# Kernel optimization log

Measured on AMD Instinct MI355X. Metric: run time of the kernel, lower is better.

Reference implementation:

```python
import jax, jax.numpy as jnp
import numpy as np
import math

NUM_HEADS = 8
HEAD_DIM = 64
MID = NUM_HEADS * HEAD_DIM  # 512
OUT_FEATURES = 512
NUM_BUCKETS = 32            # rel_pos_num_buckets (module passes 2*this to bucket fn)
MAX_DISTANCE = 128
SCALE = HEAD_DIM ** -0.5


def _relative_position_bucket(rel_pos, num_buckets, max_distance):
    # faithful port of RelativePositionBias._relative_position_bucket
    num_buckets = num_buckets // 2
    ret = (rel_pos >= 0).astype(jnp.int32) * num_buckets
    n = jnp.abs(rel_pos)
    max_exact = max(1, num_buckets // 2)
    denom = math.log(max_distance / max_exact) if max_distance > max_exact else 1.0
    n_float = jnp.maximum(n.astype(jnp.float32), 1.0)
    val_if_large = (max_exact + jnp.log(n_float / max_exact) / denom * (num_buckets - max_exact)).astype(jnp.int32)
    val_if_large = jnp.minimum(val_if_large, num_buckets - 1)
    ret = ret + jnp.where(n < max_exact, n, val_if_large)
    return ret


def rel_pos_bias(table, num_q, num_k):
    # table: [2*NUM_BUCKETS, heads] -> bias [1, heads, q, k]
    q_pos = jnp.arange(num_q, dtype=jnp.int32)
    k_pos = jnp.arange(num_k, dtype=jnp.int32)
    rel = k_pos[None, :] - q_pos[:, None]                      # [q, k]
    bucket = _relative_position_bucket(rel, NUM_BUCKETS * 2, MAX_DISTANCE)
    bias = table[bucket]                                       # [q, k, h]
    return jnp.transpose(bias, (2, 0, 1))[None]                # [1, h, q, k]


def setup_inputs() -> dict:
    key = jax.random.key(0)
    ks = jax.random.split(key, 6)
    b, n = 2, 4096
    q = jax.random.normal(ks[0], (b, n, MID), dtype=jnp.float32)
    k = jax.random.normal(ks[1], (b, n, MID), dtype=jnp.float32)
    v = jax.random.normal(ks[2], (b, n, MID), dtype=jnp.float32)
    # bucket indices range over [0, 2*NUM_BUCKETS); size table accordingly
    rel_bias_table = jax.random.normal(ks[3], (2 * NUM_BUCKETS, NUM_HEADS), dtype=jnp.float32) * 0.02
    W_out = jax.random.normal(ks[4], (MID, OUT_FEATURES), dtype=jnp.float32) * (1.0 / math.sqrt(MID))
    b_out = jax.random.normal(ks[5], (OUT_FEATURES,), dtype=jnp.float32) * 0.01
    return {"q": q, "k": k, "v": v, "rel_bias_table": rel_bias_table, "W_out": W_out, "b_out": b_out}


def reference(q, k, v, rel_bias_table, W_out, b_out):
    b, n, _ = q.shape
    m = k.shape[1]
    split = lambda t: jnp.transpose(t.reshape(t.shape[0], t.shape[1], NUM_HEADS, HEAD_DIM), (0, 2, 1, 3))
    qh, kh, vh = split(q), split(k), split(v)                  # [b, h, n, d]
    sim = jnp.einsum('bhnd,bhmd->bhnm', qh, kh)                # [b, h, n, m]
    sim = sim + rel_pos_bias(rel_bias_table, n, m)             # bias added BEFORE scaling (as in source)
    sim = sim * SCALE
    attn = jax.nn.softmax(sim, axis=-1)
    out = jnp.einsum('bhnm,bhmd->bhnd', attn, vh)              # [b, h, n, d]
    out = jnp.transpose(out, (0, 2, 1, 3)).reshape(b, n, MID)  # [b, n, h*d]
    return out @ W_out + b_out
```

## Files before the change

kernel.cpp:

```cpp
#include <hip/hip_runtime.h>
#include <hip/hip_bf16.h>
#include <math.h>

#define BB 2
#define HH 8
#define NN 4096
#define DD 64
#define MID 512
#define NOUT 512
#define QB 128
#define KVT 64
#define NT (NN / KVT)
#define LOG2E 1.44269504088896340736f
#define SCALE 0.125f

typedef __attribute__((ext_vector_type(8)))  short bf16x8;
typedef __attribute__((ext_vector_type(4)))  float f32x4;
typedef __attribute__((ext_vector_type(16))) float f32x16;

__device__ __forceinline__ short f2bf(float x) {
  unsigned u = __builtin_bit_cast(unsigned, x);
  u = (u + 0x7FFFu + ((u >> 16) & 1u)) >> 16;
  return (short)u;
}

__device__ __forceinline__ int rp_bucket(int rel) {
  int ret = (rel >= 0) ? 32 : 0;
  int n = (rel >= 0) ? rel : -rel;
  if (n < 16) return ret + n;
  float nf = (float)n;
  float vf = 16.0f + (logf(nf * (1.0f / 16.0f)) / 2.0794415416798357f) * 16.0f;
  int vi = (int)vf;
  vi = vi < 31 ? vi : 31;
  return ret + vi;
}

__device__ __forceinline__ unsigned cvtpk(float lo, float hi) {
  unsigned d;
  asm("v_cvt_pk_bf16_f32 %0, %1, %2" : "=v"(d) : "v"(lo), "v"(hi));
  return d;
}

__device__ __forceinline__ void gl2lds16(const void* g, void* l) {
  __builtin_amdgcn_global_load_lds(
      (const __attribute__((address_space(1))) unsigned*)g,
      (__attribute__((address_space(3))) unsigned*)l, 16, 0, 0);
}

__global__ void wconv_kernel(const float* __restrict__ W, short* __restrict__ Wt) {
  int i = blockIdx.x * 256 + threadIdx.x;
  int kin = i >> 9, n = i & 511;
  Wt[n * MID + kin] = f2bf(W[i]);
}

__global__ __launch_bounds__(256) void kconv_kernel(const float* __restrict__ K,
                                                    short* __restrict__ Kws) {
  int i = blockIdx.x * 256 + threadIdx.x;
  int a = i & 7;
  int h = (i >> 3) & 7;
  int n = (i >> 6) & 4095;
  int b = i >> 18;
  const float* src = K + ((size_t)(b * 4096 + n) * 512 + h * 64 + a * 8);
  float4 x0 = *(const float4*)src;
  float4 x1 = *(const float4*)(src + 4);
  union { short s[8]; bf16x8 v; } pk;
  pk.s[0] = f2bf(x0.x); pk.s[1] = f2bf(x0.y); pk.s[2] = f2bf(x0.z); pk.s[3] = f2bf(x0.w);
  pk.s[4] = f2bf(x1.x); pk.s[5] = f2bf(x1.y); pk.s[6] = f2bf(x1.z); pk.s[7] = f2bf(x1.w);
  size_t off = ((size_t)(b * 8 + h) * 4096 + n) * 64 + (size_t)((a ^ (n & 7)) * 8);
  *(bf16x8*)(Kws + off) = pk.v;
}

__global__ __launch_bounds__(256) void vconv_kernel(const float* __restrict__ V,
                                                    short* __restrict__ Vtws) {
  __shared__ short Vl[64][72];
  const int t = threadIdx.x;
  const int g = blockIdx.x;
  const int bh = blockIdx.y;
  const int b = bh >> 3, h = bh & 7;
  const int c4 = t & 15, r = t >> 4;
  #pragma unroll
  for (int rr = 0; rr < 4; ++rr) {
    int nl = r + rr * 16;
    const float* src = V + ((size_t)(b * 4096 + g * 64 + nl) * 512 + h * 64 + c4 * 4);
    float4 x = *(const float4*)src;
    Vl[nl][c4 * 4 + 0] = f2bf(x.x);
    Vl[nl][c4 * 4 + 1] = f2bf(x.y);
    Vl[nl][c4 * 4 + 2] = f2bf(x.z);
    Vl[nl][c4 * 4 + 3] = f2bf(x.w);
  }
  __syncthreads();
  #pragma unroll
  for (int it = 0; it < 2; ++it) {
    int u = t + it * 256;
    int d = u >> 3, sp = u & 7;
    int s = sp ^ (d & 7);
    union { short s[8]; bf16x8 v; } pk;
    #pragma unroll
    for (int e = 0; e < 8; ++e) {
      int np  = s * 8 + e;
      int p16 = np & 15;
      int kvl = (np & 48) | (4 * (p16 >> 3) + (p16 & 3) + 8 * ((p16 >> 2) & 1));
      pk.s[e] = Vl[kvl][d];
    }
    *(bf16x8*)(Vtws + ((size_t)bh * 64 + d) * 4096 + g * 64 + sp * 8) = pk.v;
  }
}

__global__ __launch_bounds__(256, 2) void attn_kernel(
    const float* __restrict__ q, const short* __restrict__ kws,
    const short* __restrict__ vtws, const float* __restrict__ table,
    short* __restrict__ attn_out)
{
  __shared__ short Ks[2][4096];
  __shared__ short Vs[2][4096];
  __shared__ float biasb[512];
  __shared__ float Lw[4][32];

  const int tid = threadIdx.x;
  const int w   = tid >> 6;
  const int l   = tid & 63;
  const int lq  = l & 31;
  const int hi  = l >> 5;

  const int raw = blockIdx.x;
  const int bh  = (raw & 7) * 2 + (raw >> 8);
  const int xb  = (raw >> 3) & 31;
  const int b = bh >> 3, h = bh & 7;
  const int q0 = xb * QB;
  const int qw = q0 + w * 32;
  const int qg = qw + lq;

  const float smul = SCALE * LOG2E;

  for (int i = tid; i < 512; i += 256)
    biasb[i] = table[rp_bucket(i - 256) * HH + h] * smul;
  const float c_lo = table[31 * HH + h] * smul;
  const float c_hi = table[63 * HH + h] * smul;

  f32x16 c16h, c16l;
  #pragma unroll
  for (int r = 0; r < 16; ++r) { c16h[r] = c_hi; c16l[r] = c_lo; }

  bf16x8 qf[4];
  {
    const float* qr = q + ((size_t)b * NN + qg) * MID + (size_t)h * DD;
    #pragma unroll
    for (int dc = 0; dc < 4; ++dc) {
      int d0 = dc * 16 + hi * 8;
      float4 a0 = *(const float4*)(qr + d0);
      float4 a1 = *(const float4*)(qr + d0 + 4);
      bf16x8 f;
      f[0] = f2bf(a0.x * smul); f[1] = f2bf(a0.y * smul);
      f[2] = f2bf(a0.z * smul); f[3] = f2bf(a0.w * smul);
      f[4] = f2bf(a1.x * smul); f[5] = f2bf(a1.y * smul);
      f[6] = f2bf(a1.z * smul); f[7] = f2bf(a1.w * smul);
      qf[dc] = f;
    }
  }

  const short* kbh = kws  + (size_t)bh * NN * DD;
  const short* vbh = vtws + (size_t)bh * DD * NN;

  f32x16 o0a = {}, o0b = {}, o1a = {}, o1b = {};
  float ls0 = 0.f, ls1 = 0.f, ls2 = 0.f, ls3 = 0.f;

  const int o1w = w * 1024 + l * 16;
  const int o2w = o1w + 4096;
  const char* pkA = (const char*)kbh + o1w;
  const char* pvA = (const char*)vbh + (size_t)(o1w >> 7) * 8192 + (o1w & 127);
  const char* pvB = (const char*)vbh + (size_t)(o2w >> 7) * 8192 + (o2w & 127);
  char* ldsK = (char*)&Ks[0][0] + w * 1024;
  char* ldsV = (char*)&Vs[0][0] + w * 1024;

#define STAGE(BOFF) {                                   \
    gl2lds16(pkA,        ldsK + (BOFF));                \
    gl2lds16(pkA + 4096, ldsK + (BOFF) + 4096);         \
    gl2lds16(pvA,        ldsV + (BOFF));                \
    gl2lds16(pvB,        ldsV + (BOFF) + 4096);         \
    pkA += 8192; pvA += 128; pvB += 128; }

  STAGE(0);
  __syncthreads();

  for (int t = 0; t < NT; ++t) {
    const int cur = t & 1;
    const int kv0 = t * KVT;
    if (t + 1 < NT) STAGE((cur ^ 1) ? 8192 : 0);

    const char* kr0 = (const char*)&Ks[cur][0] + lq * 128;
    const char* kr1 = kr0 + 32 * 128;
    const int swz = lq & 7;
    bf16x8 kf00 = *(const bf16x8*)(kr0 + ((hi ^ swz) << 4));
    bf16x8 kf10 = *(const bf16x8*)(kr1 + ((hi ^ swz) << 4));

    const int lo_rel = kv0 - (qw + 31);
    const int hi_rel = kv0 + KVT - 1 - qw;
    f32x16 acc0, acc1;
    if (lo_rel > 127) {
      acc0 = __builtin_amdgcn_mfma_f32_32x32x16_bf16(kf00, qf[0], c16h, 0, 0, 0);
      acc1 = __builtin_amdgcn_mfma_f32_32x32x16_bf16(kf10, qf[0], c16h, 0, 0, 0);
    } else if (hi_rel < -127) {
      acc0 = __builtin_amdgcn_mfma_f32_32x32x16_bf16(kf00, qf[0], c16l, 0, 0, 0);
      acc1 = __builtin_amdgcn_mfma_f32_32x32x16_bf16(kf10, qf[0], c16l, 0, 0, 0);
    } else {
      const int bidx0 = kv0 - qg + 256;
      f32x16 g0, g1;
      #pragma unroll
      for (int r = 0; r < 16; ++r) {
        int cr = (r & 3) + 8 * (r >> 2) + 4 * hi;
        g0[r] = biasb[bidx0 + cr];
        g1[r] = biasb[bidx0 + 32 + cr];
      }
      acc0 = __builtin_amdgcn_mfma_f32_32x32x16_bf16(kf00, qf[0], g0, 0, 0, 0);
      acc1 = __builtin_amdgcn_mfma_f32_32x32x16_bf16(kf10, qf[0], g1, 0, 0, 0);
    }
    __builtin_amdgcn_s_setprio(1);
    #pragma unroll
    for (int dc = 1; dc < 4; ++dc) {
      bf16x8 kf0 = *(const bf16x8*)(kr0 + (((dc * 2 + hi) ^ swz) << 4));
      bf16x8 kf1 = *(const bf16x8*)(kr1 + (((dc * 2 + hi) ^ swz) << 4));
      acc0 = __builtin_amdgcn_mfma_f32_32x32x16_bf16(kf0, qf[dc], acc0, 0, 0, 0);
      acc1 = __builtin_amdgcn_mfma_f32_32x32x16_bf16(kf1, qf[dc], acc1, 0, 0, 0);
    }
    __builtin_amdgcn_s_setprio(0);

    float p0[16], p1[16];
    #pragma unroll
    for (int r = 0; r < 16; ++r) p0[r] = __builtin_amdgcn_exp2f(acc0[r]);
    #pragma unroll
    for (int r = 0; r < 16; ++r) p1[r] = __builtin_amdgcn_exp2f(acc1[r]);

    ls0 += ((p0[0] + p0[1]) + (p0[2] + p0[3])) + ((p0[4] + p0[5]) + (p0[6] + p0[7]));
    ls1 += ((p0[8] + p0[9]) + (p0[10] + p0[11])) + ((p0[12] + p0[13]) + (p0[14] + p0[15]));
    ls2 += ((p1[0] + p1[1]) + (p1[2] + p1[3])) + ((p1[4] + p1[5]) + (p1[6] + p1[7]));
    ls3 += ((p1[8] + p1[9]) + (p1[10] + p1[11])) + ((p1[12] + p1[13]) + (p1[14] + p1[15]));

    bf16x8 pa[4];
    {
      union { unsigned u[4]; bf16x8 v; } ua, ub, uc, ud;
      ua.u[0] = cvtpk(p0[0],  p0[1]);  ua.u[1] = cvtpk(p0[2],  p0[3]);
      ua.u[2] = cvtpk(p0[4],  p0[5]);  ua.u[3] = cvtpk(p0[6],  p0[7]);
      ub.u[0] = cvtpk(p0[8],  p0[9]);  ub.u[1] = cvtpk(p0[10], p0[11]);
      ub.u[2] = cvtpk(p0[12], p0[13]); ub.u[3] = cvtpk(p0[14], p0[15]);
      uc.u[0] = cvtpk(p1[0],  p1[1]);  uc.u[1] = cvtpk(p1[2],  p1[3]);
      uc.u[2] = cvtpk(p1[4],  p1[5]);  uc.u[3] = cvtpk(p1[6],  p1[7]);
      ud.u[0] = cvtpk(p1[8],  p1[9]);  ud.u[1] = cvtpk(p1[10], p1[11]);
      ud.u[2] = cvtpk(p1[12], p1[13]); ud.u[3] = cvtpk(p1[14], p1[15]);
      pa[0] = ua.v; pa[1] = ub.v; pa[2] = uc.v; pa[3] = ud.v;
    }

    {
      const char* vb = (const char*)&Vs[cur][0];
      const char* vr0 = vb + lq * 128;
      const char* vr1 = vr0 + 32 * 128;
      const int s0 = lq & 7;
      __builtin_amdgcn_s_setprio(1);
      #pragma unroll
      for (int ks = 0; ks < 4; ks += 2) {
        bf16x8 vfa0 = *(const bf16x8*)(vr0 + (((hi + 2 * ks) ^ s0) << 4));
        bf16x8 vfb0 = *(const bf16x8*)(vr0 + (((hi + 2 * (ks + 1)) ^ s0) << 4));
        bf16x8 vfa1 = *(const bf16x8*)(vr1 + (((hi + 2 * ks) ^ s0) << 4));
        bf16x8 vfb1 = *(const bf16x8*)(vr1 + (((hi + 2 * (ks + 1)) ^ s0) << 4));
        o0a = __builtin_amdgcn_mfma_f32_32x32x16_bf16(pa[ks],     vfa0, o0a, 0, 0, 0);
        o0b = __builtin_amdgcn_mfma_f32_32x32x16_bf16(pa[ks + 1], vfb0, o0b, 0, 0, 0);
        o1a = __builtin_amdgcn_mfma_f32_32x32x16_bf16(pa[ks],     vfa1, o1a, 0, 0, 0);
        o1b = __builtin_amdgcn_mfma_f32_32x32x16_bf16(pa[ks + 1], vfb1, o1b, 0, 0, 0);
      }
      __builtin_amdgcn_s_setprio(0);
    }

    __syncthreads();
  }

  f32x16 o0, o1;
  #pragma unroll
  for (int r = 0; r < 16; ++r) { o0[r] = o0a[r] + o0b[r]; o1[r] = o1a[r] + o1b[r]; }
  float lsum = (ls0 + ls1) + (ls2 + ls3);
  float tot = lsum + __shfl_xor(lsum, 32);
  if (l < 32) Lw[w][l] = tot;
  float inv[16];
  #pragma unroll
  for (int g = 0; g < 4; ++g) {
    f32x4 t4 = *(const f32x4*)&Lw[w][g * 8 + hi * 4];
    inv[g * 4 + 0] = 1.0f / t4[0];
    inv[g * 4 + 1] = 1.0f / t4[1];
    inv[g * 4 + 2] = 1.0f / t4[2];
    inv[g * 4 + 3] = 1.0f / t4[3];
  }
  const size_t ob = ((size_t)b * NN + qw) * MID + (size_t)h * DD;
  #pragma unroll
  for (int r = 0; r < 16; ++r) {
    const int crow = (r & 3) + 8 * (r >> 2) + 4 * hi;
    short* orow = attn_out + ob + (size_t)crow * MID;
    orow[lq]      = f2bf(o0[r] * inv[r]);
    orow[32 + lq] = f2bf(o1[r] * inv[r]);
  }
#undef STAGE
}

__global__ __launch_bounds__(256) void proj_kernel(
    const short* __restrict__ A, const short* __restrict__ Wt,
    const float* __restrict__ bias, float* __restrict__ out)
{
  const int tid = threadIdx.x;
  const int w  = tid >> 6;
  const int l  = tid & 63;
  const int lr = l & 15;
  const int lg = l >> 4;
  const int m0 = blockIdx.x * 64 + w * 16;
  const int n0 = blockIdx.y * 64;

  f32x4 acc[4] = {};
  const short* ar = A + (size_t)(m0 + lr) * MID + lg * 8;
  #pragma unroll
  for (int kk = 0; kk < MID; kk += 32) {
    bf16x8 af = *(const bf16x8*)(ar + kk);
    #pragma unroll
    for (int u = 0; u < 4; ++u) {
      bf16x8 bfr = *(const bf16x8*)(Wt + (size_t)(n0 + u * 16 + lr) * MID + kk + lg * 8);
      acc[u] = __builtin_amdgcn_mfma_f32_16x16x32_bf16(af, bfr, acc[u], 0, 0, 0);
    }
  }
  #pragma unroll
  for (int u = 0; u < 4; ++u) {
    float bb = bias[n0 + u * 16 + lr];
    #pragma unroll
    for (int r = 0; r < 4; ++r)
      out[(size_t)(m0 + lg * 4 + r) * NOUT + n0 + u * 16 + lr] = acc[u][r] + bb;
  }
}

extern "C" void kernel_launch(void* const* d_in, const int* in_sizes, int n_in,
                              void* d_out, int out_size, void* d_ws, size_t ws_size,
                              hipStream_t stream) {
  const float* q     = (const float*)d_in[0];
  const float* k     = (const float*)d_in[1];
  const float* v     = (const float*)d_in[2];
  const float* table = (const float*)d_in[3];
  const float* W     = (const float*)d_in[4];
  const float* bo    = (const float*)d_in[5];
  float* out = (float*)d_out;

  char* wsp = (char*)d_ws;
  short* attn_ws = (short*)wsp;                       wsp += (size_t)BB * NN * MID * 2;
  short* Wt      = (short*)wsp;                       wsp += (size_t)MID * NOUT * 2;
  short* kws     = (short*)wsp;                       wsp += (size_t)BB * HH * NN * DD * 2;
  short* vtws    = (short*)wsp;

  hipLaunchKernelGGL(wconv_kernel, dim3(MID * NOUT / 256), dim3(256), 0, stream, W, Wt);
  hipLaunchKernelGGL(kconv_kernel, dim3(BB * HH * NN * DD / 8 / 256), dim3(256), 0, stream, k, kws);
  hipLaunchKernelGGL(vconv_kernel, dim3(NN / 64, BB * HH), dim3(256), 0, stream, v, vtws);
  hipLaunchKernelGGL(attn_kernel, dim3(BB * HH * (NN / QB)), dim3(256), 0, stream,
                     q, kws, vtws, table, attn_ws);
  hipLaunchKernelGGL(proj_kernel, dim3(BB * NN / 64, NOUT / 64), dim3(256), 0, stream,
                     attn_ws, Wt, bo, out);
}
```

Measured before the change: 140.4 us.

## Split KV across wave pairs with smaller query blocks and LDS reduction

Halves the query block to 64 rows, so each block has two wave pairs. Each pair handles a different 32-key half of every 64-key stage, with both pairs sharing the 32 query rows per wave. This doubles the number of blocks and raises the occupancy hint to 4 blocks per CU, with smaller per-wave accumulators. The partial outputs and row sums from the two pairs are combined through LDS at the end. The V transpose layout and its swizzle change to match the 32-key sub-tiles. In exchange, each K/V tile serves fewer query rows, so global and LDS traffic per output rises, and an extra reduction with syncs is added.

```diff
diff --git a/kernel.cpp b/kernel.cpp
--- a/kernel.cpp
+++ b/kernel.cpp
@@ -8,9 +8,9 @@
 #define DD 64
 #define MID 512
 #define NOUT 512
-#define QB 128
-#define KVT 64
-#define NT (NN / KVT)
+#define QB 64
+#define KVT 32
+#define NSS 64
 #define LOG2E 1.44269504088896340736f
 #define SCALE 0.125f
 
@@ -93,11 +93,12 @@
   for (int it = 0; it < 2; ++it) {
     int u = t + it * 256;
     int d = u >> 3, sp = u & 7;
-    int s = sp ^ (d & 7);
+    int chunk = sp >> 2;
+    int sl = (sp & 3) ^ (d & 3);
     union { short s[8]; bf16x8 v; } pk;
     #pragma unroll
     for (int e = 0; e < 8; ++e) {
-      int np  = s * 8 + e;
+      int np  = chunk * 32 + sl * 8 + e;
       int p16 = np & 15;
       int kvl = (np & 48) | (4 * (p16 >> 3) + (p16 & 3) + 8 * ((p16 >> 2) & 1));
       pk.s[e] = Vl[kvl][d];
@@ -106,13 +107,13 @@
   }
 }
 
-__global__ __launch_bounds__(256, 2) void attn_kernel(
+__global__ __launch_bounds__(256, 4) void attn_kernel(
     const float* __restrict__ q, const short* __restrict__ kws,
     const short* __restrict__ vtws, const float* __restrict__ table,
     short* __restrict__ attn_out)
 {
-  __shared__ short Ks[2][4096];
-  __shared__ short Vs[2][4096];
+  __shared__ short Ks[2][2][2048];
+  __shared__ short Vs[2][2][2048];
   __shared__ float biasb[512];
   __shared__ float Lw[4][32];
 
@@ -121,13 +122,15 @@
   const int l   = tid & 63;
   const int lq  = l & 31;
   const int hi  = l >> 5;
+  const int p   = w >> 1;
+  const int qs  = (w & 1) * 32;
 
   const int raw = blockIdx.x;
-  const int bh  = (raw & 7) * 2 + (raw >> 8);
-  const int xb  = (raw >> 3) & 31;
+  const int bh  = (raw & 7) * 2 + (raw >> 9);
+  const int xb  = (raw >> 3) & 63;
   const int b = bh >> 3, h = bh & 7;
   const int q0 = xb * QB;
-  const int qw = q0 + w * 32;
+  const int qw = q0 + qs;
   const int qg = qw + lq;
 
   const float smul = SCALE * LOG2E;
@@ -158,114 +161,87 @@
     }
   }
 
-  const short* kbh = kws  + (size_t)bh * NN * DD;
-  const short* vbh = vtws + (size_t)bh * DD * NN;
+  const char* kbh = (const char*)(kws  + (size_t)bh * NN * DD);
+  const char* vbh = (const char*)(vtws + (size_t)bh * DD * NN);
 
   f32x16 o0a = {}, o0b = {}, o1a = {}, o1b = {};
-  float ls0 = 0.f, ls1 = 0.f, ls2 = 0.f, ls3 = 0.f;
-
-  const int o1w = w * 1024 + l * 16;
-  const int o2w = o1w + 4096;
-  const char* pkA = (const char*)kbh + o1w;
-  const char* pvA = (const char*)vbh + (size_t)(o1w >> 7) * 8192 + (o1w & 127);
-  const char* pvB = (const char*)vbh + (size_t)(o2w >> 7) * 8192 + (o2w & 127);
-  char* ldsK = (char*)&Ks[0][0] + w * 1024;
-  char* ldsV = (char*)&Vs[0][0] + w * 1024;
-
-#define STAGE(BOFF) {                                   \
-    gl2lds16(pkA,        ldsK + (BOFF));                \
-    gl2lds16(pkA + 4096, ldsK + (BOFF) + 4096);         \
-    gl2lds16(pvA,        ldsV + (BOFF));                \
-    gl2lds16(pvB,        ldsV + (BOFF) + 4096);         \
-    pkA += 8192; pvA += 128; pvB += 128; }
-
-  STAGE(0);
+  float ls0 = 0.f, ls1 = 0.f;
+
+  const char* pk = kbh + tid * 16;
+  const char* pv = vbh + (size_t)(tid >> 2) * 8192 + (tid & 3) * 16;
+
+#define STAGE(BUF, SS) {                                                    \
+    gl2lds16(pk + (size_t)(SS) * 8192,        (char*)&Ks[BUF][0][0] + w * 1024); \
+    gl2lds16(pk + (size_t)(SS) * 8192 + 4096, (char*)&Ks[BUF][1][0] + w * 1024); \
+    gl2lds16(pv + (SS) * 128,                 (char*)&Vs[BUF][0][0] + w * 1024); \
+    gl2lds16(pv + (SS) * 128 + 64,            (char*)&Vs[BUF][1][0] + w * 1024); }
+
+  STAGE(0, 0);
   __syncthreads();
 
-  for (int t = 0; t < NT; ++t) {
-    const int cur = t & 1;
-    const int kv0 = t * KVT;
-    if (t + 1 < NT) STAGE((cur ^ 1) ? 8192 : 0);
-
-    const char* kr0 = (const char*)&Ks[cur][0] + lq * 128;
-    const char* kr1 = kr0 + 32 * 128;
+  for (int ss = 0; ss < NSS; ++ss) {
+    const int cur = ss & 1;
+    if (ss + 1 < NSS) STAGE(cur ^ 1, ss + 1);
+
+    const int kv0 = ss * 64 + p * 32;
+
+    const char* kr = (const char*)&Ks[cur][p][0] + lq * 128;
     const int swz = lq & 7;
-    bf16x8 kf00 = *(const bf16x8*)(kr0 + ((hi ^ swz) << 4));
-    bf16x8 kf10 = *(const bf16x8*)(kr1 + ((hi ^ swz) << 4));
+    bf16x8 kf0 = *(const bf16x8*)(kr + ((hi ^ swz) << 4));
 
     const int lo_rel = kv0 - (qw + 31);
     const int hi_rel = kv0 + KVT - 1 - qw;
-    f32x16 acc0, acc1;
+    f32x16 acc;
     if (lo_rel > 127) {
-      acc0 = __builtin_amdgcn_mfma_f32_32x32x16_bf16(kf00, qf[0], c16h, 0, 0, 0);
-      acc1 = __builtin_amdgcn_mfma_f32_32x32x16_bf16(kf10, qf[0], c16h, 0, 0, 0);
+      acc = __builtin_amdgcn_mfma_f32_32x32x16_bf16(kf0, qf[0], c16h, 0, 0, 0);
     } else if (hi_rel < -127) {
-      acc0 = __builtin_amdgcn_mfma_f32_32x32x16_bf16(kf00, qf[0], c16l, 0, 0, 0);
-      acc1 = __builtin_amdgcn_mfma_f32_32x32x16_bf16(kf10, qf[0], c16l, 0, 0, 0);
+      acc = __builtin_amdgcn_mfma_f32_32x32x16_bf16(kf0, qf[0], c16l, 0, 0, 0);
     } else {
       const int bidx0 = kv0 - qg + 256;
-      f32x16 g0, g1;
+      f32x16 g0;
       #pragma unroll
-      for (int r = 0; r < 16; ++r) {
-        int cr = (r & 3) + 8 * (r >> 2) + 4 * hi;
-        g0[r] = biasb[bidx0 + cr];
-        g1[r] = biasb[bidx0 + 32 + cr];
-      }
-      acc0 = __builtin_amdgcn_mfma_f32_32x32x16_bf16(kf00, qf[0], g0, 0, 0, 0);
-      acc1 = __builtin_amdgcn_mfma_f32_32x32x16_bf16(kf10, qf[0], g1, 0, 0, 0);
+      for (int r = 0; r < 16; ++r)
+        g0[r] = biasb[bidx0 + ((r & 3) + 8 * (r >> 2) + 4 * hi)];
+      acc = __builtin_amdgcn_mfma_f32_32x32x16_bf16(kf0, qf[0], g0, 0, 0, 0);
     }
     __builtin_amdgcn_s_setprio(1);
     #pragma unroll
     for (int dc = 1; dc < 4; ++dc) {
-      bf16x8 kf0 = *(const bf16x8*)(kr0 + (((dc * 2 + hi) ^ swz) << 4));
-      bf16x8 kf1 = *(const bf16x8*)(kr1 + (((dc * 2 + hi) ^ swz) << 4));
-      acc0 = __builtin_amdgcn_mfma_f32_32x32x16_bf16(kf0, qf[dc], acc0, 0, 0, 0);
-      acc1 = __builtin_amdgcn_mfma_f32_32x32x16_bf16(kf1, qf[dc], acc1, 0, 0, 0);
+      bf16x8 kf = *(const bf16x8*)(kr + (((dc * 2 + hi) ^ swz) << 4));
+      acc = __builtin_amdgcn_mfma_f32_32x32x16_bf16(kf, qf[dc], acc, 0, 0, 0);
     }
     __builtin_amdgcn_s_setprio(0);
 
-    float p0[16], p1[16];
-    #pragma unroll
-    for (int r = 0; r < 16; ++r) p0[r] = __builtin_amdgcn_exp2f(acc0[r]);
-    #pragma unroll
-    for (int r = 0; r < 16; ++r) p1[r] = __builtin_amdgcn_exp2f(acc1[r]);
-
+    float p0[16];
+    #pragma unroll
+    for (int r = 0; r < 16; ++r) p0[r] = __builtin_amdgcn_exp2f(acc[r]);
     ls0 += ((p0[0] + p0[1]) + (p0[2] + p0[3])) + ((p0[4] + p0[5]) + (p0[6] + p0[7]));
     ls1 += ((p0[8] + p0[9]) + (p0[10] + p0[11])) + ((p0[12] + p0[13]) + (p0[14] + p0[15]));
-    ls2 += ((p1[0] + p1[1]) + (p1[2] + p1[3])) + ((p1[4] + p1[5]) + (p1[6] + p1[7]));
-    ls3 += ((p1[8] + p1[9]) + (p1[10] + p1[11])) + ((p1[12] + p1[13]) + (p1[14] + p1[15]));
-
-    bf16x8 pa[4];
+
+    bf16x8 pa0, pa1;
     {
-      union { unsigned u[4]; bf16x8 v; } ua, ub, uc, ud;
+      union { unsigned u[4]; bf16x8 v; } ua, ub;
       ua.u[0] = cvtpk(p0[0],  p0[1]);  ua.u[1] = cvtpk(p0[2],  p0[3]);
       ua.u[2] = cvtpk(p0[4],  p0[5]);  ua.u[3] = cvtpk(p0[6],  p0[7]);
       ub.u[0] = cvtpk(p0[8],  p0[9]);  ub.u[1] = cvtpk(p0[10], p0[11]);
       ub.u[2] = cvtpk(p0[12], p0[13]); ub.u[3] = cvtpk(p0[14], p0[15]);
-      uc.u[0] = cvtpk(p1[0],  p1[1]);  uc.u[1] = cvtpk(p1[2],  p1[3]);
-      uc.u[2] = cvtpk(p1[4],  p1[5]);  uc.u[3] = cvtpk(p1[6],  p1[7]);
-      ud.u[0] = cvtpk(p1[8],  p1[9]);  ud.u[1] = cvtpk(p1[10], p1[11]);
-      ud.u[2] = cvtpk(p1[12], p1[13]); ud.u[3] = cvtpk(p1[14], p1[15]);
-      pa[0] = ua.v; pa[1] = ub.v; pa[2] = uc.v; pa[3] = ud.v;
+      pa0 = ua.v; pa1 = ub.v;
     }
 
     {
-      const char* vb = (const char*)&Vs[cur][0];
-      const char* vr0 = vb + lq * 128;
-      const char* vr1 = vr0 + 32 * 128;
-      const int s0 = lq & 7;
+      const char* vb  = (const char*)&Vs[cur][p][0];
+      const char* vr0 = vb + lq * 64;
+      const char* vr1 = vb + (32 + lq) * 64;
+      const int s0 = lq & 3;
       __builtin_amdgcn_s_setprio(1);
-      #pragma unroll
-      for (int ks = 0; ks < 4; ks += 2) {
-        bf16x8 vfa0 = *(const bf16x8*)(vr0 + (((hi + 2 * ks) ^ s0) << 4));
-        bf16x8 vfb0 = *(const bf16x8*)(vr0 + (((hi + 2 * (ks + 1)) ^ s0) << 4));
-        bf16x8 vfa1 = *(const bf16x8*)(vr1 + (((hi + 2 * ks) ^ s0) << 4));
-        bf16x8 vfb1 = *(const bf16x8*)(vr1 + (((hi + 2 * (ks + 1)) ^ s0) << 4));
-        o0a = __builtin_amdgcn_mfma_f32_32x32x16_bf16(pa[ks],     vfa0, o0a, 0, 0, 0);
-        o0b = __builtin_amdgcn_mfma_f32_32x32x16_bf16(pa[ks + 1], vfb0, o0b, 0, 0, 0);
-        o1a = __builtin_amdgcn_mfma_f32_32x32x16_bf16(pa[ks],     vfa1, o1a, 0, 0, 0);
-        o1b = __builtin_amdgcn_mfma_f32_32x32x16_bf16(pa[ks + 1], vfb1, o1b, 0, 0, 0);
-      }
+      bf16x8 va0 = *(const bf16x8*)(vr0 + ((hi ^ s0) << 4));
+      bf16x8 vb0 = *(const bf16x8*)(vr0 + (((hi + 2) ^ s0) << 4));
+      bf16x8 va1 = *(const bf16x8*)(vr1 + ((hi ^ s0) << 4));
+      bf16x8 vb1 = *(const bf16x8*)(vr1 + (((hi + 2) ^ s0) << 4));
+      o0a = __builtin_amdgcn_mfma_f32_32x32x16_bf16(pa0, va0, o0a, 0, 0, 0);
+      o0b = __builtin_amdgcn_mfma_f32_32x32x16_bf16(pa1, vb0, o0b, 0, 0, 0);
+      o1a = __builtin_amdgcn_mfma_f32_32x32x16_bf16(pa0, va1, o1a, 0, 0, 0);
+      o1b = __builtin_amdgcn_mfma_f32_32x32x16_bf16(pa1, vb1, o1b, 0, 0, 0);
       __builtin_amdgcn_s_setprio(0);
     }
 
@@ -275,25 +251,42 @@
   f32x16 o0, o1;
   #pragma unroll
   for (int r = 0; r < 16; ++r) { o0[r] = o0a[r] + o0b[r]; o1[r] = o1a[r] + o1b[r]; }
-  float lsum = (ls0 + ls1) + (ls2 + ls3);
+  float lsum = ls0 + ls1;
   float tot = lsum + __shfl_xor(lsum, 32);
   if (l < 32) Lw[w][l] = tot;
-  float inv[16];
-  #pragma unroll
-  for (int g = 0; g < 4; ++g) {
-    f32x4 t4 = *(const f32x4*)&Lw[w][g * 8 + hi * 4];
-    inv[g * 4 + 0] = 1.0f / t4[0];
-    inv[g * 4 + 1] = 1.0f / t4[1];
-    inv[g * 4 + 2] = 1.0f / t4[2];
-    inv[g * 4 + 3] = 1.0f / t4[3];
-  }
-  const size_t ob = ((size_t)b * NN + qw) * MID + (size_t)h * DD;
-  #pragma unroll
-  for (int r = 0; r < 16; ++r) {
-    const int crow = (r & 3) + 8 * (r >> 2) + 4 * hi;
-    short* orow = attn_out + ob + (size_t)crow * MID;
-    orow[lq]      = f2bf(o0[r] * inv[r]);
-    orow[32 + lq] = f2bf(o1[r] * inv[r]);
+
+  float* Olds = (float*)&Ks[0][0][0];
+  __syncthreads();
+  if (w >= 2) {
+    float* ob = Olds + (w & 1) * 2048;
+    #pragma unroll
+    for (int r = 0; r < 16; ++r) {
+      const int crow = (r & 3) + 8 * (r >> 2) + 4 * hi;
+      ob[crow * 64 + lq]      = o0[r];
+      ob[crow * 64 + 32 + lq] = o1[r];
+    }
+  }
+  __syncthreads();
+  if (w < 2) {
+    float inv[16];
+    #pragma unroll
+    for (int g = 0; g < 4; ++g) {
+      f32x4 ta = *(const f32x4*)&Lw[w][g * 8 + hi * 4];
+      f32x4 tb = *(const f32x4*)&Lw[w + 2][g * 8 + hi * 4];
+      inv[g * 4 + 0] = 1.0f / (ta[0] + tb[0]);
+      inv[g * 4 + 1] = 1.0f / (ta[1] + tb[1]);
+      inv[g * 4 + 2] = 1.0f / (ta[2] + tb[2]);
+      inv[g * 4 + 3] = 1.0f / (ta[3] + tb[3]);
+    }
+    const float* ob = Olds + (w & 1) * 2048;
+    const size_t obase = ((size_t)b * NN + qw) * MID + (size_t)h * DD;
+    #pragma unroll
+    for (int r = 0; r < 16; ++r) {
+      const int crow = (r & 3) + 8 * (r >> 2) + 4 * hi;
+      short* orow = attn_out + obase + (size_t)crow * MID;
+      orow[lq]      = f2bf((o0[r] + ob[crow * 64 + lq])      * inv[r]);
+      orow[32 + lq] = f2bf((o1[r] + ob[crow * 64 + 32 + lq]) * inv[r]);
+    }
   }
 #undef STAGE
 }
```

Result: slower. 444.7 us (+216.8%).

## Triple-buffer K/V tiles with one barrier per step and fuse prep kernels

Applied to the files above, without the earlier changes.

The attention loop moves from double to triple buffering of K/V tiles in LDS. It waits with explicit vmcnt counts and uses a single barrier per iteration, while the load for tile t+2 is issued after compute. The three conversion kernels (W transpose, K swizzle, V transpose) are merged into one launch dispatched by block index, cutting launch overhead. The cost is 16 KB more LDS per block, which may reduce occupancy from the two blocks per CU requested by the launch bounds. It also relies on the hand-written vmcnt accounting being right.

```diff
diff --git a/kernel.cpp b/kernel.cpp
--- a/kernel.cpp
+++ b/kernel.cpp
@@ -47,62 +47,64 @@
       (__attribute__((address_space(3))) unsigned*)l, 16, 0, 0);
 }
 
-__global__ void wconv_kernel(const float* __restrict__ W, short* __restrict__ Wt) {
-  int i = blockIdx.x * 256 + threadIdx.x;
-  int kin = i >> 9, n = i & 511;
-  Wt[n * MID + kin] = f2bf(W[i]);
-}
-
-__global__ __launch_bounds__(256) void kconv_kernel(const float* __restrict__ K,
-                                                    short* __restrict__ Kws) {
-  int i = blockIdx.x * 256 + threadIdx.x;
-  int a = i & 7;
-  int h = (i >> 3) & 7;
-  int n = (i >> 6) & 4095;
-  int b = i >> 18;
-  const float* src = K + ((size_t)(b * 4096 + n) * 512 + h * 64 + a * 8);
-  float4 x0 = *(const float4*)src;
-  float4 x1 = *(const float4*)(src + 4);
-  union { short s[8]; bf16x8 v; } pk;
-  pk.s[0] = f2bf(x0.x); pk.s[1] = f2bf(x0.y); pk.s[2] = f2bf(x0.z); pk.s[3] = f2bf(x0.w);
-  pk.s[4] = f2bf(x1.x); pk.s[5] = f2bf(x1.y); pk.s[6] = f2bf(x1.z); pk.s[7] = f2bf(x1.w);
-  size_t off = ((size_t)(b * 8 + h) * 4096 + n) * 64 + (size_t)((a ^ (n & 7)) * 8);
-  *(bf16x8*)(Kws + off) = pk.v;
-}
-
-__global__ __launch_bounds__(256) void vconv_kernel(const float* __restrict__ V,
-                                                    short* __restrict__ Vtws) {
-  __shared__ short Vl[64][72];
-  const int t = threadIdx.x;
-  const int g = blockIdx.x;
-  const int bh = blockIdx.y;
-  const int b = bh >> 3, h = bh & 7;
-  const int c4 = t & 15, r = t >> 4;
-  #pragma unroll
-  for (int rr = 0; rr < 4; ++rr) {
-    int nl = r + rr * 16;
-    const float* src = V + ((size_t)(b * 4096 + g * 64 + nl) * 512 + h * 64 + c4 * 4);
-    float4 x = *(const float4*)src;
-    Vl[nl][c4 * 4 + 0] = f2bf(x.x);
-    Vl[nl][c4 * 4 + 1] = f2bf(x.y);
-    Vl[nl][c4 * 4 + 2] = f2bf(x.z);
-    Vl[nl][c4 * 4 + 3] = f2bf(x.w);
-  }
-  __syncthreads();
-  #pragma unroll
-  for (int it = 0; it < 2; ++it) {
-    int u = t + it * 256;
-    int d = u >> 3, sp = u & 7;
-    int s = sp ^ (d & 7);
+__global__ __launch_bounds__(256) void prep_kernel(
+    const float* __restrict__ W,  short* __restrict__ Wt,
+    const float* __restrict__ K,  short* __restrict__ Kws,
+    const float* __restrict__ V,  short* __restrict__ Vtws)
+{
+  const int bx = blockIdx.x;
+  const int t  = threadIdx.x;
+  if (bx < 2048) {
+    int i = bx * 256 + t;
+    int a = i & 7;
+    int h = (i >> 3) & 7;
+    int n = (i >> 6) & 4095;
+    int b = i >> 18;
+    const float* src = K + ((size_t)(b * 4096 + n) * 512 + h * 64 + a * 8);
+    float4 x0 = *(const float4*)src;
+    float4 x1 = *(const float4*)(src + 4);
     union { short s[8]; bf16x8 v; } pk;
-    #pragma unroll
-    for (int e = 0; e < 8; ++e) {
-      int np  = s * 8 + e;
-      int p16 = np & 15;
-      int kvl = (np & 48) | (4 * (p16 >> 3) + (p16 & 3) + 8 * ((p16 >> 2) & 1));
-      pk.s[e] = Vl[kvl][d];
-    }
-    *(bf16x8*)(Vtws + ((size_t)bh * 64 + d) * 4096 + g * 64 + sp * 8) = pk.v;
+    pk.s[0] = f2bf(x0.x); pk.s[1] = f2bf(x0.y); pk.s[2] = f2bf(x0.z); pk.s[3] = f2bf(x0.w);
+    pk.s[4] = f2bf(x1.x); pk.s[5] = f2bf(x1.y); pk.s[6] = f2bf(x1.z); pk.s[7] = f2bf(x1.w);
+    size_t off = ((size_t)(b * 8 + h) * 4096 + n) * 64 + (size_t)((a ^ (n & 7)) * 8);
+    *(bf16x8*)(Kws + off) = pk.v;
+  } else if (bx < 3072) {
+    __shared__ short Vl[64][72];
+    const int idx = bx - 2048;
+    const int g = idx & 63;
+    const int bh = idx >> 6;
+    const int b = bh >> 3, h = bh & 7;
+    const int c4 = t & 15, r = t >> 4;
+    #pragma unroll
+    for (int rr = 0; rr < 4; ++rr) {
+      int nl = r + rr * 16;
+      const float* src = V + ((size_t)(b * 4096 + g * 64 + nl) * 512 + h * 64 + c4 * 4);
+      float4 x = *(const float4*)src;
+      Vl[nl][c4 * 4 + 0] = f2bf(x.x);
+      Vl[nl][c4 * 4 + 1] = f2bf(x.y);
+      Vl[nl][c4 * 4 + 2] = f2bf(x.z);
+      Vl[nl][c4 * 4 + 3] = f2bf(x.w);
+    }
+    __syncthreads();
+    #pragma unroll
+    for (int it = 0; it < 2; ++it) {
+      int u = t + it * 256;
+      int d = u >> 3, sp = u & 7;
+      int s = sp ^ (d & 7);
+      union { short s[8]; bf16x8 v; } pk;
+      #pragma unroll
+      for (int e = 0; e < 8; ++e) {
+        int np  = s * 8 + e;
+        int p16 = np & 15;
+        int kvl = (np & 48) | (4 * (p16 >> 3) + (p16 & 3) + 8 * ((p16 >> 2) & 1));
+        pk.s[e] = Vl[kvl][d];
+      }
+      *(bf16x8*)(Vtws + ((size_t)bh * 64 + d) * 4096 + g * 64 + sp * 8) = pk.v;
+    }
+  } else {
+    int i = (bx - 3072) * 256 + t;
+    int kin = i >> 9, n = i & 511;
+    Wt[n * MID + kin] = f2bf(W[i]);
   }
 }
 
@@ -111,8 +113,8 @@
     const short* __restrict__ vtws, const float* __restrict__ table,
     short* __restrict__ attn_out)
 {
-  __shared__ short Ks[2][4096];
-  __shared__ short Vs[2][4096];
+  __shared__ short Ks[3][4096];
+  __shared__ short Vs[3][4096];
   __shared__ float biasb[512];
   __shared__ float Lw[4][32];
 
@@ -171,6 +173,8 @@
   const char* pvB = (const char*)vbh + (size_t)(o2w >> 7) * 8192 + (o2w & 127);
   char* ldsK = (char*)&Ks[0][0] + w * 1024;
   char* ldsV = (char*)&Vs[0][0] + w * 1024;
+  const char* kbase = (const char*)&Ks[0][0];
+  const char* vbase = (const char*)&Vs[0][0];
 
 #define STAGE(BOFF) {                                   \
     gl2lds16(pkA,        ldsK + (BOFF));                \
@@ -179,15 +183,20 @@
     gl2lds16(pvB,        ldsV + (BOFF) + 4096);         \
     pkA += 8192; pvA += 128; pvB += 128; }
 
+  __syncthreads();
   STAGE(0);
-  __syncthreads();
+  STAGE(8192);
+
+  int bo_cur = 0, bo_nxt = 16384;
 
   for (int t = 0; t < NT; ++t) {
-    const int cur = t & 1;
+    if (t + 1 < NT) asm volatile("s_waitcnt vmcnt(4)" ::: "memory");
+    else            asm volatile("s_waitcnt vmcnt(0)" ::: "memory");
+    __builtin_amdgcn_s_barrier();
+
     const int kv0 = t * KVT;
-    if (t + 1 < NT) STAGE((cur ^ 1) ? 8192 : 0);
-
-    const char* kr0 = (const char*)&Ks[cur][0] + lq * 128;
+
+    const char* kr0 = kbase + bo_cur + lq * 128;
     const char* kr1 = kr0 + 32 * 128;
     const int swz = lq & 7;
     bf16x8 kf00 = *(const bf16x8*)(kr0 + ((hi ^ swz) << 4));
@@ -250,8 +259,7 @@
     }
 
     {
-      const char* vb = (const char*)&Vs[cur][0];
-      const char* vr0 = vb + lq * 128;
+      const char* vr0 = vbase + bo_cur + lq * 128;
       const char* vr1 = vr0 + 32 * 128;
       const int s0 = lq & 7;
       __builtin_amdgcn_s_setprio(1);
@@ -269,7 +277,9 @@
       __builtin_amdgcn_s_setprio(0);
     }
 
-    __syncthreads();
+    if (t + 2 < NT) STAGE(bo_nxt);
+    bo_cur = (bo_cur == 16384) ? 0 : bo_cur + 8192;
+    bo_nxt = (bo_nxt == 16384) ? 0 : bo_nxt + 8192;
   }
 
   f32x16 o0, o1;
@@ -278,6 +288,7 @@
   float lsum = (ls0 + ls1) + (ls2 + ls3);
   float tot = lsum + __shfl_xor(lsum, 32);
   if (l < 32) Lw[w][l] = tot;
+  __syncthreads();
   float inv[16];
   #pragma unroll
   for (int g = 0; g < 4; ++g) {
@@ -347,9 +358,8 @@
   short* kws     = (short*)wsp;                       wsp += (size_t)BB * HH * NN * DD * 2;
   short* vtws    = (short*)wsp;
 
-  hipLaunchKernelGGL(wconv_kernel, dim3(MID * NOUT / 256), dim3(256), 0, stream, W, Wt);
-  hipLaunchKernelGGL(kconv_kernel, dim3(BB * HH * NN * DD / 8 / 256), dim3(256), 0, stream, k, kws);
-  hipLaunchKernelGGL(vconv_kernel, dim3(NN / 64, BB * HH), dim3(256), 0, stream, v, vtws);
+  hipLaunchKernelGGL(prep_kernel, dim3(4096), dim3(256), 0, stream,
+                     W, Wt, k, kws, v, vtws);
   hipLaunchKernelGGL(attn_kernel, dim3(BB * HH * (NN / QB)), dim3(256), 0, stream,
                      q, kws, vtws, table, attn_ws);
   hipLaunchKernelGGL(proj_kernel, dim3(BB * NN / 64, NOUT / 64), dim3(256), 0, stream,
```

New measurement: 132.7 us. 5.5% less time.
